# Kernel tuning notes

Measured on AMD Instinct MI355X. Metric: run time of the kernel, lower is better.

Reference implementation:

```python
import jax, jax.numpy as jnp
import numpy as np

P = 64          # batch_size * grad_accumulation_steps (perturbation population)
OUT = 1024
IN = 1024


def setup_inputs() -> dict:
    key = jax.random.key(0)
    k = jax.random.split(key, 6)
    return {
        "x": jax.random.normal(k[0], (8, 2048, IN), dtype=jnp.float32),
        "weight": jax.random.normal(k[1], (OUT, IN), dtype=jnp.float32) * 0.02,
        "bias": jax.random.normal(k[2], (OUT,), dtype=jnp.float32) * 0.02,
        "scale": jax.random.normal(k[3], (P,), dtype=jnp.float32) * 0.01,
        "weight_perturbations": jax.random.normal(k[4], (P, OUT, IN), dtype=jnp.float16),
        "bias_perturbations": jax.random.normal(k[5], (P, OUT), dtype=jnp.float16),
    }


def reference(x, weight, bias, scale, weight_perturbations, bias_perturbations):
    # fp16 -> fp32 upcast then scale-weighted reduction over population dim i
    w = weight + jnp.einsum("i,ijk->jk", scale, weight_perturbations.astype(jnp.float32))
    b = bias + jnp.einsum("i,ij->j", scale, bias_perturbations.astype(jnp.float32))
    # F.linear(x, w, b) == x @ w.T + b
    return jnp.einsum("bsk,jk->bsj", x, w) + b
```

## Files before the change

### kernel.cpp

```cpp
#include <hip/hip_runtime.h>
#include <hip/hip_bf16.h>
#include <hip/hip_fp16.h>

#define PPOP 64
#define NOUT 1024
#define KIN  1024
#define MROWS (8*2048)

typedef __bf16 bf16x8 __attribute__((ext_vector_type(8)));
typedef __bf16 bf16x4 __attribute__((ext_vector_type(4)));
typedef float  f32x4  __attribute__((ext_vector_type(4)));
typedef unsigned short u16x8 __attribute__((ext_vector_type(8)));

#define GLOAD_LDS16(gp, lp)                                                  \
  __builtin_amdgcn_global_load_lds(                                          \
      (const __attribute__((address_space(1))) void*)(gp),                   \
      (__attribute__((address_space(3))) void*)(lp), 16, 0, 0)

__device__ __forceinline__ float dec_bf16u(unsigned short u) {
  union { unsigned u32; float f; } c; c.u32 = ((unsigned)u) << 16; return c.f;
}
__device__ __forceinline__ float dec_f16u(unsigned short u) {
  union { unsigned short s; __half h; } c; c.s = u; return __half2float(c.h);
}

#define DK 2048
struct DetectArgs {
  const void* p[6];
  long n[6];
  float target[6];
  int* flags;
};

__global__ __launch_bounds__(256) void detect_kernel(DetectArgs a) {
  __shared__ float ssum[3], ssq[3];
  __shared__ int sbad[3];
  const int t = blockIdx.x;
  const unsigned short* h = (const unsigned short*)a.p[t];
  const float* f = (const float*)a.p[t];
  const long n = a.n[t];
  const long half_n = n >> 1;
  if (threadIdx.x < 3) { ssum[threadIdx.x] = 0.f; ssq[threadIdx.x] = 0.f; sbad[threadIdx.x] = 0; }
  __syncthreads();

  float lsum[3] = {0.f, 0.f, 0.f}, lsq[3] = {0.f, 0.f, 0.f};
  int lbad[3] = {0, 0, 0};
  for (int j = threadIdx.x; j < DK; j += 256) {
    const long idx  = ((long)j * n) / DK;
    const long idx2 = ((long)j * half_n) / DK;
    const unsigned short u = h[idx];
    float vv[3];
    vv[0] = f[idx2];
    vv[1] = dec_bf16u(u);
    vv[2] = dec_f16u(u);
#pragma unroll
    for (int d = 0; d < 3; ++d) {
      const float av = fabsf(vv[d]);
      if (!isfinite(av) || av == 0.f) { lbad[d]++; }
      else { const float l = log2f(av); lsum[d] += l; lsq[d] += l * l; }
    }
  }
#pragma unroll
  for (int d = 0; d < 3; ++d) {
    atomicAdd(&ssum[d], lsum[d]); atomicAdd(&ssq[d], lsq[d]); atomicAdd(&sbad[d], lbad[d]);
  }
  __syncthreads();
  if (threadIdx.x == 0) {
    int flag = 0;
    const float tgt = a.target[t];
    for (int d = 1; d <= 2; ++d) {
      const int cnt = DK - sbad[d];
      if (sbad[d] == 0 && cnt > 0) {
        const float m = ssum[d] / cnt;
        const float var = ssq[d] / cnt - m * m;
        if (var > 1.0f && var < 6.5f && fabsf(m - tgt) < 3.0f) { flag = d; break; }
      }
    }
    a.flags[t] = flag;
  }
}

#define XCONV_BLK0 513
#define XCONV_NBLK (MROWS * KIN / (256 * 8))

__global__ __launch_bounds__(256) void prep_adaptive(
    const void* __restrict__ x,      const void* __restrict__ weight,
    const void* __restrict__ bias,   const void* __restrict__ scale,
    const void* __restrict__ wp,     const void* __restrict__ bp,
    __bf16* __restrict__ wout,       float* __restrict__ bout,
    __bf16* __restrict__ xout,       const int* __restrict__ flags)
{
  const int b = blockIdx.x;

  if (b >= XCONV_BLK0) {
    const int fx = flags[0];
    if (fx == 1) return;
    const long e = ((long)(b - XCONV_BLK0) * 256 + threadIdx.x) * 8;
    bf16x8 o;
    if (fx == 0) {
      const float* xf = (const float*)x + e;
      const float4 v0 = ((const float4*)xf)[0];
      const float4 v1 = ((const float4*)xf)[1];
      o[0] = (__bf16)v0.x; o[1] = (__bf16)v0.y; o[2] = (__bf16)v0.z; o[3] = (__bf16)v0.w;
      o[4] = (__bf16)v1.x; o[5] = (__bf16)v1.y; o[6] = (__bf16)v1.z; o[7] = (__bf16)v1.w;
    } else {
      const u16x8 v = *(const u16x8*)((const unsigned short*)x + e);
#pragma unroll
      for (int t = 0; t < 8; ++t) o[t] = (__bf16)dec_f16u(v[t]);
    }
    *(bf16x8*)(xout + e) = o;
    return;
  }

  const int fw = flags[1], fb = flags[2], fs = flags[3], fwp = flags[4], fbp = flags[5];
  __shared__ float s[PPOP];
  if (threadIdx.x < PPOP) {
    float v;
    if (fs == 0)      v = ((const float*)scale)[threadIdx.x];
    else if (fs == 1) v = dec_bf16u(((const unsigned short*)scale)[threadIdx.x]);
    else              v = dec_f16u(((const unsigned short*)scale)[threadIdx.x]);
    s[threadIdx.x] = v;
  }
  __syncthreads();

  if (b < 512) {
    const int c = b * 256 + threadIdx.x;
    const long e = (long)c * 8;
    float acc[8];
    if (fw == 0) {
      const float4 w0 = ((const float4*)((const float*)weight + e))[0];
      const float4 w1 = ((const float4*)((const float*)weight + e))[1];
      acc[0] = w0.x; acc[1] = w0.y; acc[2] = w0.z; acc[3] = w0.w;
      acc[4] = w1.x; acc[5] = w1.y; acc[6] = w1.z; acc[7] = w1.w;
    } else {
      const u16x8 w = *(const u16x8*)((const unsigned short*)weight + e);
#pragma unroll
      for (int t = 0; t < 8; ++t)
        acc[t] = (fw == 1) ? dec_bf16u(w[t]) : dec_f16u(w[t]);
    }
    if (fwp == 0) {
      const float* wpf = (const float*)wp;
#pragma unroll 4
      for (int i = 0; i < PPOP; ++i) {
        const float4 p0 = ((const float4*)(wpf + (long)i * (NOUT * KIN) + e))[0];
        const float4 p1 = ((const float4*)(wpf + (long)i * (NOUT * KIN) + e))[1];
        const float sc = s[i];
        acc[0] += sc * p0.x; acc[1] += sc * p0.y; acc[2] += sc * p0.z; acc[3] += sc * p0.w;
        acc[4] += sc * p1.x; acc[5] += sc * p1.y; acc[6] += sc * p1.z; acc[7] += sc * p1.w;
      }
    } else if (fwp == 1) {
      const unsigned short* wph = (const unsigned short*)wp;
#pragma unroll 8
      for (int i = 0; i < PPOP; ++i) {
        const u16x8 p = *(const u16x8*)(wph + (long)i * (NOUT * KIN) + e);
        const float sc = s[i];
#pragma unroll
        for (int t = 0; t < 8; ++t) acc[t] += sc * dec_bf16u(p[t]);
      }
    } else {
      const unsigned short* wph = (const unsigned short*)wp;
#pragma unroll 8
      for (int i = 0; i < PPOP; ++i) {
        const u16x8 p = *(const u16x8*)(wph + (long)i * (NOUT * KIN) + e);
        const float sc = s[i];
#pragma unroll
        for (int t = 0; t < 8; ++t) acc[t] += sc * dec_f16u(p[t]);
      }
    }
    bf16x8 o;
#pragma unroll
    for (int t = 0; t < 8; ++t) o[t] = (__bf16)acc[t];
    *(bf16x8*)(wout + e) = o;
  } else {
#pragma unroll
    for (int t = 0; t < 4; ++t) {
      const int j = t * 256 + threadIdx.x;
      float a;
      if (fb == 0)      a = ((const float*)bias)[j];
      else if (fb == 1) a = dec_bf16u(((const unsigned short*)bias)[j]);
      else              a = dec_f16u(((const unsigned short*)bias)[j]);
      if (fbp == 0) {
        const float* bpf = (const float*)bp;
        for (int i = 0; i < PPOP; ++i) a += s[i] * bpf[i * NOUT + j];
      } else if (fbp == 1) {
        const unsigned short* bph = (const unsigned short*)bp;
        for (int i = 0; i < PPOP; ++i) a += s[i] * dec_bf16u(bph[i * NOUT + j]);
      } else {
        const unsigned short* bph = (const unsigned short*)bp;
        for (int i = 0; i < PPOP; ++i) a += s[i] * dec_f16u(bph[i * NOUT + j]);
      }
      bout[j] = a;
    }
  }
}

__global__ __launch_bounds__(256) void gemm_bf16(
    const void* __restrict__ X, const __bf16* __restrict__ Xc,
    const __bf16* __restrict__ Wb, const float* __restrict__ Bv,
    float* __restrict__ out, const int* __restrict__ flags)
{
  __shared__ __bf16 As[128 * 32];
  __shared__ __bf16 Bs[128 * 32];

  const __bf16* Xb = (flags[0] == 1) ? (const __bf16*)X : Xc;

  const int tid  = threadIdx.x;
  const int lane = tid & 63;
  const int wave = tid >> 6;
  const int wm   = (wave >> 1) * 64;
  const int wn   = (wave & 1) * 64;
  const int q    = lane >> 4;
  const int r16  = lane & 15;
  const int cm   = blockIdx.y * 128;
  const int cn   = blockIdx.x * 128;

  const __bf16* ga = Xb + (long)(cm + (tid >> 2)) * KIN + (tid & 3) * 8;
  const __bf16* gb = Wb + (long)(cn + (tid >> 2)) * KIN + (tid & 3) * 8;

  f32x4 acc[4][4] = {};

  for (int k0 = 0; k0 < KIN; k0 += 32) {
    if (k0) __syncthreads();

    GLOAD_LDS16(ga + k0,            As + tid * 8);
    GLOAD_LDS16(ga + 64 * KIN + k0, As + (256 + tid) * 8);
    GLOAD_LDS16(gb + k0,            Bs + tid * 8);
    GLOAD_LDS16(gb + 64 * KIN + k0, Bs + (256 + tid) * 8);

    __syncthreads();

    const bf16x8* Ap = (const bf16x8*)As;
    const bf16x8* Bp = (const bf16x8*)Bs;
    bf16x8 af[4], bfr[4];
#pragma unroll
    for (int mt = 0; mt < 4; ++mt) af[mt]  = Ap[(wm + mt * 16 + r16) * 4 + q];
#pragma unroll
    for (int nt = 0; nt < 4; ++nt) bfr[nt] = Bp[(wn + nt * 16 + r16) * 4 + q];
#pragma unroll
    for (int mt = 0; mt < 4; ++mt)
#pragma unroll
      for (int nt = 0; nt < 4; ++nt)
        acc[mt][nt] = __builtin_amdgcn_mfma_f32_16x16x32_bf16(
            af[mt], bfr[nt], acc[mt][nt], 0, 0, 0);
  }

  float bv[4];
#pragma unroll
  for (int nt = 0; nt < 4; ++nt) bv[nt] = Bv[cn + wn + nt * 16 + r16];

#pragma unroll
  for (int mt = 0; mt < 4; ++mt)
#pragma unroll
    for (int nt = 0; nt < 4; ++nt) {
      const int n = cn + wn + nt * 16 + r16;
#pragma unroll
      for (int r = 0; r < 4; ++r) {
        const int m = cm + wm + mt * 16 + q * 4 + r;
        out[(long)m * NOUT + n] = acc[mt][nt][r] + bv[nt];
      }
    }
}

extern "C" void kernel_launch(void* const* d_in, const int* in_sizes, int n_in,
                              void* d_out, int out_size, void* d_ws, size_t ws_size,
                              hipStream_t stream) {
  const void *x = nullptr, *weight = nullptr, *bias = nullptr,
             *scale = nullptr, *wp = nullptr, *bp = nullptr;
  for (int i = 0; i < n_in; ++i) {
    switch (in_sizes[i]) {
      case 16777216: x      = d_in[i]; break;
      case 1048576:  weight = d_in[i]; break;
      case 1024:     bias   = d_in[i]; break;
      case 64:       scale  = d_in[i]; break;
      case 67108864: wp     = d_in[i]; break;
      case 65536:    bp     = d_in[i]; break;
      default: break;
    }
  }
  if (!x || !weight || !bias || !scale || !wp || !bp) return;

  __bf16* wb   = (__bf16*)d_ws;
  float*  bb   = (float*)((char*)d_ws + (size_t)2 * 1024 * 1024);
  int*    flag = (int*)((char*)d_ws + (size_t)2 * 1024 * 1024 + 4096);
  __bf16* xb   = (__bf16*)((char*)d_ws + (size_t)4 * 1024 * 1024);
  float*  out  = (float*)d_out;

  DetectArgs da;
  da.p[0] = x;      da.n[0] = 16777216; da.target[0] = -0.92f;
  da.p[1] = weight; da.n[1] = 1048576;  da.target[1] = -6.56f;
  da.p[2] = bias;   da.n[2] = 1024;     da.target[2] = -6.56f;
  da.p[3] = scale;  da.n[3] = 64;       da.target[3] = -7.56f;
  da.p[4] = wp;     da.n[4] = 67108864; da.target[4] = -0.92f;
  da.p[5] = bp;     da.n[5] = 65536;    da.target[5] = -0.92f;
  da.flags = flag;

  detect_kernel<<<6, 256, 0, stream>>>(da);
  prep_adaptive<<<XCONV_BLK0 + XCONV_NBLK, 256, 0, stream>>>(
      x, weight, bias, scale, wp, bp, wb, bb, xb, flag);
  dim3 grid(NOUT / 128, MROWS / 128);
  gemm_bf16<<<grid, 256, 0, stream>>>(x, xb, wb, bb, out, flag);
}
```

Baseline: 504.7 us.

## Replace 128x128 GEMM with double-buffered 256x256 eight-wave phased pipeline

Replaces the single-buffered 128x128x32 bf16 GEMM with a 256x256x64 tile kernel using 512 threads, double-buffered LDS with an XOR swizzle, and a four-phase schedule that interleaves global-to-LDS prefetch of the next K tile with MFMA work on the current one. It also remaps block ids so neighbouring blocks share input tiles, and raises wave priority around the MFMA clusters. The aim is to hide memory latency, cut LDS bank conflicts and raise arithmetic intensity. In exchange it uses 128 KB of LDS per block and many more registers, which limits occupancy, and it adds manual barriers whose correctness is subtle.

```diff
diff --git a/kernel.cpp b/kernel.cpp
--- a/kernel.cpp
+++ b/kernel.cpp
@@ -194,71 +194,169 @@
   }
 }
 
-__global__ __launch_bounds__(256) void gemm_bf16(
+#define BM 256
+#define BN 256
+#define BK 64
+#define NT_K (KIN / BK)
+
+__global__ __launch_bounds__(512, 2) void gemm_8phase(
     const void* __restrict__ X, const __bf16* __restrict__ Xc,
     const __bf16* __restrict__ Wb, const float* __restrict__ Bv,
     float* __restrict__ out, const int* __restrict__ flags)
 {
-  __shared__ __bf16 As[128 * 32];
-  __shared__ __bf16 Bs[128 * 32];
+  __shared__ __bf16 lds[2][2][BM * BK];
 
   const __bf16* Xb = (flags[0] == 1) ? (const __bf16*)X : Xc;
+
+  const int bid = blockIdx.x;
+  const int wg  = (bid & 7) * 32 + (bid >> 3);
+  const int cm  = (wg >> 2) * BM;
+  const int cn  = (wg & 3) * BN;
 
   const int tid  = threadIdx.x;
   const int lane = tid & 63;
   const int wave = tid >> 6;
-  const int wm   = (wave >> 1) * 64;
-  const int wn   = (wave & 1) * 64;
+  const int wm   = (wave >> 2) * 128;
+  const int wn   = (wave & 3) * 64;
   const int q    = lane >> 4;
   const int r16  = lane & 15;
-  const int cm   = blockIdx.y * 128;
-  const int cn   = blockIdx.x * 128;
-
-  const __bf16* ga = Xb + (long)(cm + (tid >> 2)) * KIN + (tid & 3) * 8;
-  const __bf16* gb = Wb + (long)(cn + (tid >> 2)) * KIN + (tid & 3) * 8;
-
-  f32x4 acc[4][4] = {};
-
-  for (int k0 = 0; k0 < KIN; k0 += 32) {
-    if (k0) __syncthreads();
-
-    GLOAD_LDS16(ga + k0,            As + tid * 8);
-    GLOAD_LDS16(ga + 64 * KIN + k0, As + (256 + tid) * 8);
-    GLOAD_LDS16(gb + k0,            Bs + tid * 8);
-    GLOAD_LDS16(gb + 64 * KIN + k0, Bs + (256 + tid) * 8);
-
-    __syncthreads();
-
-    const bf16x8* Ap = (const bf16x8*)As;
-    const bf16x8* Bp = (const bf16x8*)Bs;
-    bf16x8 af[4], bfr[4];
-#pragma unroll
-    for (int mt = 0; mt < 4; ++mt) af[mt]  = Ap[(wm + mt * 16 + r16) * 4 + q];
-#pragma unroll
-    for (int nt = 0; nt < 4; ++nt) bfr[nt] = Bp[(wn + nt * 16 + r16) * 4 + q];
-#pragma unroll
-    for (int mt = 0; mt < 4; ++mt)
-#pragma unroll
-      for (int nt = 0; nt < 4; ++nt)
-        acc[mt][nt] = __builtin_amdgcn_mfma_f32_16x16x32_bf16(
-            af[mt], bfr[nt], acc[mt][nt], 0, 0, 0);
-  }
-
-  float bv[4];
-#pragma unroll
-  for (int nt = 0; nt < 4; ++nt) bv[nt] = Bv[cn + wn + nt * 16 + r16];
-
-#pragma unroll
-  for (int mt = 0; mt < 4; ++mt)
-#pragma unroll
-    for (int nt = 0; nt < 4; ++nt) {
-      const int n = cn + wn + nt * 16 + r16;
-#pragma unroll
-      for (int r = 0; r < 4; ++r) {
-        const int m = cm + wm + mt * 16 + q * 4 + r;
-        out[(long)m * NOUT + n] = acc[mt][nt][r] + bv[nt];
-      }
-    }
+  const int sw   = r16 & 7;
+
+  const __bf16* gA = Xb + (long)cm * KIN;
+  const __bf16* gB = Wb + (long)cn * KIN;
+
+  auto STAGE = [&](__bf16* ldst, const __bf16* gsrc, int h, int kt) {
+#pragma unroll
+    for (int it = 0; it < 2; ++it) {
+      const int c  = tid + it * 512;
+      const int rr = (h << 7) + (c >> 3);
+      const int kc = ((((c & 7) ^ ((c >> 3) & 7))) << 3) + (kt << 6);
+      GLOAD_LDS16(gsrc + (long)rr * KIN + kc, ldst + ((h << 10) + c) * 8);
+    }
+  };
+
+  f32x4 acc[8][4] = {};
+  bf16x8 af[2][4], b0[2][2], b1[2][2];
+
+  STAGE(&lds[0][0][0], gA, 0, 0);
+  STAGE(&lds[0][0][0], gA, 1, 0);
+  STAGE(&lds[0][1][0], gB, 0, 0);
+  STAGE(&lds[0][1][0], gB, 1, 0);
+  asm volatile("s_waitcnt vmcnt(0)" ::: "memory");
+  __builtin_amdgcn_s_barrier();
+
+#pragma unroll 2
+  for (int t = 0; t < NT_K; ++t) {
+    const int cur = t & 1;
+    const int nxt = cur ^ 1;
+    const bool pf = (t + 1 < NT_K);
+    const __bf16* pa = &lds[cur][0][0];
+    const __bf16* pb = &lds[cur][1][0];
+
+#pragma unroll
+    for (int mt = 0; mt < 4; ++mt) {
+      const int o = (wm + mt * 16 + r16) * 64 + ((q ^ sw) << 3);
+      af[0][mt] = *(const bf16x8*)(pa + o);
+      af[1][mt] = *(const bf16x8*)(pa + (o ^ 32));
+    }
+#pragma unroll
+    for (int nt = 0; nt < 2; ++nt) {
+      const int o = (wn + nt * 16 + r16) * 64 + ((q ^ sw) << 3);
+      b0[0][nt] = *(const bf16x8*)(pb + o);
+      b0[1][nt] = *(const bf16x8*)(pb + (o ^ 32));
+    }
+    if (pf) STAGE(&lds[nxt][0][0], gA, 0, t + 1);
+    __builtin_amdgcn_s_barrier();
+    asm volatile("s_waitcnt lgkmcnt(0)" ::: "memory");
+    __builtin_amdgcn_sched_barrier(0);
+    __builtin_amdgcn_s_setprio(1);
+#pragma unroll
+    for (int kk = 0; kk < 2; ++kk)
+#pragma unroll
+      for (int mt = 0; mt < 4; ++mt)
+#pragma unroll
+        for (int nt = 0; nt < 2; ++nt)
+          acc[mt][nt] = __builtin_amdgcn_mfma_f32_16x16x32_bf16(
+              af[kk][mt], b0[kk][nt], acc[mt][nt], 0, 0, 0);
+    __builtin_amdgcn_s_setprio(0);
+    __builtin_amdgcn_s_barrier();
+
+#pragma unroll
+    for (int nt = 0; nt < 2; ++nt) {
+      const int o = (wn + 32 + nt * 16 + r16) * 64 + ((q ^ sw) << 3);
+      b1[0][nt] = *(const bf16x8*)(pb + o);
+      b1[1][nt] = *(const bf16x8*)(pb + (o ^ 32));
+    }
+    if (pf) STAGE(&lds[nxt][0][0], gA, 1, t + 1);
+    __builtin_amdgcn_s_barrier();
+    asm volatile("s_waitcnt lgkmcnt(0)" ::: "memory");
+    __builtin_amdgcn_sched_barrier(0);
+    __builtin_amdgcn_s_setprio(1);
+#pragma unroll
+    for (int kk = 0; kk < 2; ++kk)
+#pragma unroll
+      for (int mt = 0; mt < 4; ++mt)
+#pragma unroll
+        for (int nt = 0; nt < 2; ++nt)
+          acc[mt][2 + nt] = __builtin_amdgcn_mfma_f32_16x16x32_bf16(
+              af[kk][mt], b1[kk][nt], acc[mt][2 + nt], 0, 0, 0);
+    __builtin_amdgcn_s_setprio(0);
+    __builtin_amdgcn_s_barrier();
+
+#pragma unroll
+    for (int mt = 0; mt < 4; ++mt) {
+      const int o = (wm + 64 + mt * 16 + r16) * 64 + ((q ^ sw) << 3);
+      af[0][mt] = *(const bf16x8*)(pa + o);
+      af[1][mt] = *(const bf16x8*)(pa + (o ^ 32));
+    }
+    if (pf) STAGE(&lds[nxt][1][0], gB, 0, t + 1);
+    __builtin_amdgcn_s_barrier();
+    asm volatile("s_waitcnt lgkmcnt(0)" ::: "memory");
+    __builtin_amdgcn_sched_barrier(0);
+    __builtin_amdgcn_s_setprio(1);
+#pragma unroll
+    for (int kk = 0; kk < 2; ++kk)
+#pragma unroll
+      for (int mt = 0; mt < 4; ++mt)
+#pragma unroll
+        for (int nt = 0; nt < 2; ++nt)
+          acc[4 + mt][2 + nt] = __builtin_amdgcn_mfma_f32_16x16x32_bf16(
+              af[kk][mt], b1[kk][nt], acc[4 + mt][2 + nt], 0, 0, 0);
+    __builtin_amdgcn_s_setprio(0);
+    __builtin_amdgcn_s_barrier();
+
+    if (pf) STAGE(&lds[nxt][1][0], gB, 1, t + 1);
+    __builtin_amdgcn_s_barrier();
+    asm volatile("s_waitcnt lgkmcnt(0)" ::: "memory");
+    __builtin_amdgcn_s_setprio(1);
+#pragma unroll
+    for (int kk = 0; kk < 2; ++kk)
+#pragma unroll
+      for (int mt = 0; mt < 4; ++mt)
+#pragma unroll
+        for (int nt = 0; nt < 2; ++nt)
+          acc[4 + mt][nt] = __builtin_amdgcn_mfma_f32_16x16x32_bf16(
+              af[kk][mt], b0[kk][nt], acc[4 + mt][nt], 0, 0, 0);
+    __builtin_amdgcn_s_setprio(0);
+    if (pf) asm volatile("s_waitcnt vmcnt(0)" ::: "memory");
+    __builtin_amdgcn_s_barrier();
+  }
+
+  float bvv[4];
+#pragma unroll
+  for (int bn = 0; bn < 4; ++bn) bvv[bn] = Bv[cn + wn + bn * 16 + r16];
+
+#pragma unroll
+  for (int a = 0; a < 8; ++a) {
+    const long mrow = (long)(cm + wm + a * 16 + q * 4);
+#pragma unroll
+    for (int bn = 0; bn < 4; ++bn) {
+      const int n = cn + wn + bn * 16 + r16;
+#pragma unroll
+      for (int r = 0; r < 4; ++r)
+        out[(mrow + r) * NOUT + n] = acc[a][bn][r] + bvv[bn];
+    }
+  }
 }
 
 extern "C" void kernel_launch(void* const* d_in, const int* in_sizes, int n_in,
@@ -297,6 +395,6 @@
   detect_kernel<<<6, 256, 0, stream>>>(da);
   prep_adaptive<<<XCONV_BLK0 + XCONV_NBLK, 256, 0, stream>>>(
       x, weight, bias, scale, wp, bp, wb, bb, xb, flag);
-  dim3 grid(NOUT / 128, MROWS / 128);
-  gemm_bf16<<<grid, 256, 0, stream>>>(x, xb, wb, bb, out, flag);
-}
+  gemm_8phase<<<dim3((MROWS / BM) * (NOUT / BN)), 512, 0, stream>>>(
+      x, xb, wb, bb, out, flag);
+}
```

New measurement: 483.6 us. 4.2% less time.
